# Kernel tuning notes

Measured on AMD Instinct MI355X. Metric: run time of the kernel, lower is better.

## Reference

```python
import jax, jax.numpy as jnp
import numpy as np

B, L, D = 4, 4096, 1024
H = 16
DK = D // H  # 64
EPS = 1e-5


def setup_inputs() -> dict:
    key = jax.random.key(0)
    ks = jax.random.split(key, 9)
    s = 1.0 / np.sqrt(D)
    return {
        "Q": jax.random.normal(ks[0], (B, L, D), dtype=jnp.float32),
        "W_Q": jax.random.uniform(ks[1], (D, D), jnp.float32, -s, s),
        "b_Q": jax.random.uniform(ks[2], (D,), jnp.float32, -s, s),
        "W_K": jax.random.uniform(ks[3], (D, D), jnp.float32, -s, s),
        "b_K": jax.random.uniform(ks[4], (D,), jnp.float32, -s, s),
        "W_V": jax.random.uniform(ks[5], (D, D), jnp.float32, -s, s),
        "b_V": jax.random.uniform(ks[6], (D,), jnp.float32, -s, s),
        "W_O": jax.random.uniform(ks[7], (D, D), jnp.float32, -s, s),
        "b_O": jax.random.uniform(ks[8], (D,), jnp.float32, -s, s),
    }


def reference(Q, W_Q, b_Q, W_K, b_K, W_V, b_V, W_O, b_O):
    # Projections (torch Linear: x @ W.T + b). K = V = Q (self-attention).
    q = (Q @ W_Q.T + b_Q).reshape(B, L, H, DK)  # blhd
    k = (Q @ W_K.T + b_K).reshape(B, L, H, DK)
    v = (Q @ W_V.T + b_V).reshape(B, L, H, DK)

    phi_q = jax.nn.elu(q) + 1.0
    phi_k = jax.nn.elu(k) + 1.0

    # KV outer-product accumulation over sequence: [b,h,d,m]
    KV = jnp.einsum('blhd,blhm->bhdm', phi_k, v)
    K_sum = phi_k.sum(axis=1)                       # [b,h,d]
    Z = 1.0 / (jnp.einsum('blhd,bhd->blh', phi_q, K_sum) + EPS)
    V_new = jnp.einsum('blhd,bhdm->blhm', phi_q, KV) * Z[..., None]

    out = V_new.reshape(B, L, H * DK) @ W_O.T + b_O  # [b,L,d_model]
    return out
```

## Files before the change

kernel.cpp:

```cpp
#include <hip/hip_runtime.h>

typedef unsigned short u16;
typedef unsigned int   u32;
typedef __attribute__((ext_vector_type(8))) short short8;
typedef __attribute__((ext_vector_type(4))) float f32x4;
typedef __attribute__((ext_vector_type(4))) u16   u16x4;

#define NB 4
#define SL 4096
#define DM 1024
#define NH 16
#define DK 64

__device__ __forceinline__ u16 f2bf(float f) {
  u32 u = __builtin_bit_cast(u32, f);
  u = (u + 0x7fffu + ((u >> 16) & 1u)) >> 16;
  return (u16)u;
}
__device__ __forceinline__ float bf2f(u16 v) {
  u32 u = ((u32)v) << 16;
  return __builtin_bit_cast(float, u);
}
__device__ __forceinline__ float eluP1(float x) {
  return x > 0.f ? x + 1.f : __expf(x);
}
#define GLL(gp, lp) __builtin_amdgcn_global_load_lds(     \
    (const __attribute__((address_space(1))) void*)(gp),  \
    (__attribute__((address_space(3))) void*)(lp), 16, 0, 0)

__global__ void cvt_all(const float* __restrict__ Qf,
                        const float* __restrict__ WQ, const float* __restrict__ WK,
                        const float* __restrict__ WV, const float* __restrict__ WO,
                        const float* __restrict__ bQ, const float* __restrict__ bK,
                        const float* __restrict__ bV,
                        u16* __restrict__ Qbf, u16* __restrict__ Wqkv,
                        u16* __restrict__ Wobf, float* __restrict__ biasQKV) {
  int b = blockIdx.x, tid = threadIdx.x;
  if (b < 16384) {
    int i = b * 256 + tid;
    f32x4 f = *(const f32x4*)(Qf + (size_t)i * 4);
    u16x4 o = { f2bf(f[0]), f2bf(f[1]), f2bf(f[2]), f2bf(f[3]) };
    *(u16x4*)(Qbf + (size_t)i * 4) = o;
  } else if (b < 20480) {
    int r = (b - 16384) >> 10;
    int i = ((b - 16384) & 1023) * 256 + tid;
    const float* src = r == 0 ? WQ : r == 1 ? WK : r == 2 ? WV : WO;
    u16* dst = (r == 3) ? Wobf : Wqkv + (size_t)r * 1048576;
    f32x4 f = *(const f32x4*)(src + (size_t)i * 4);
    u16x4 o = { f2bf(f[0]), f2bf(f[1]), f2bf(f[2]), f2bf(f[3]) };
    *(u16x4*)(dst + (size_t)i * 4) = o;
  } else {
    int i = (b - 20480) * 256 + tid;
    if (i < 3072) {
      float v = (i < 1024) ? bQ[i] : (i < 2048) ? bK[i - 1024] : bV[i - 2048];
      biasQKV[i] = v;
    }
  }
}


#define VM8 asm volatile("s_waitcnt vmcnt(8)" ::: "memory")

#define SA(buf, ks, kt) do {                                      \
    const u16* g_ = Ag + (((kt) & 15) * 64 + (ks) * 32);          \
    u16* l_ = ldsA + (buf) * 32768 + (ks) * 8192;                 \
    GLL(g_, l_); GLL(g_ + 16 * 1024, l_ + 512); } while (0)

#define SB(buf, ks, kt) do {                                      \
    const u16* g_ = Wg + (((kt) & 15) * 64 + (ks) * 32);          \
    u16* l_ = ldsB + (buf) * 32768 + (ks) * 8192;                 \
    GLL(g_, l_); GLL(g_ + 16 * 1024, l_ + 512); } while (0)

#define RD4(SET, buf, ks) do {                                    \
    const u16* pA_ = aBase + (buf) * 32768 + (ks) * 8192;         \
    _Pragma("unroll") for (int t_ = 0; t_ < 4; t_++)              \
      SET[t_] = *(const short8*)(pA_ + aOff[4 + t_]); } while (0)

#define RD8(ASET, BSET, buf, ks) do {                             \
    const u16* pA_ = aBase + (buf) * 32768 + (ks) * 8192;         \
    const u16* pB_ = bBase + (buf) * 32768 + (ks) * 8192;         \
    _Pragma("unroll") for (int t_ = 0; t_ < 4; t_++)              \
      ASET[t_] = *(const short8*)(pA_ + aOff[t_]);                \
    _Pragma("unroll") for (int u_ = 0; u_ < 4; u_++)              \
      BSET[u_] = *(const short8*)(pB_ + bOff[u_]); } while (0)

#define MFMA16(AF, BF, tb)                                        \
    _Pragma("unroll") for (int t_ = 0; t_ < 4; t_++) {            \
      acc[(tb) + t_][0] = __builtin_amdgcn_mfma_f32_16x16x32_bf16(AF[t_], BF[0], acc[(tb) + t_][0], 0, 0, 0); \
      acc[(tb) + t_][1] = __builtin_amdgcn_mfma_f32_16x16x32_bf16(AF[t_], BF[1], acc[(tb) + t_][1], 0, 0, 0); \
      acc[(tb) + t_][2] = __builtin_amdgcn_mfma_f32_16x16x32_bf16(AF[t_], BF[2], acc[(tb) + t_][2], 0, 0, 0); \
      acc[(tb) + t_][3] = __builtin_amdgcn_mfma_f32_16x16x32_bf16(AF[t_], BF[3], acc[(tb) + t_][3], 0, 0, 0); \
    }

#define PH(AFC, BFC, tb, RDOP, N, STG) do {                       \
    RDOP;                                                         \
    asm volatile("s_waitcnt lgkmcnt(" #N ")" ::: "memory");       \
    __builtin_amdgcn_sched_barrier(0);                            \
    __builtin_amdgcn_s_setprio(1);                                \
    MFMA16(AFC, BFC, tb);                                         \
    __builtin_amdgcn_s_setprio(0);                                \
    STG;                                                          \
    VM8;                                                          \
    __builtin_amdgcn_s_barrier();                                 \
  } while (0)

#define MAIN_8PHASE_LOOP                                          \
  short8 afA[4], afB[4], bfX[4], bfY[4];                          \
  SA(0, 0, 0); SB(0, 0, 0); SA(0, 1, 0); SB(0, 1, 0);             \
  SA(1, 0, 1); SB(1, 0, 1); SB(1, 1, 1);                          \
  VM8;                                                            \
  __builtin_amdgcn_s_barrier();                                   \
  asm volatile("" ::: "memory");                                  \
  RD8(afA, bfX, 0, 0);                                            \
  _Pragma("unroll 1")                                             \
  for (int i = 0; i < 8; i++) {                                   \
    PH(afA, bfX, 0, RD4(afB, 0, 0),        4, SA(1, 1, 2 * i + 1)); \
    PH(afB, bfX, 4, RD8(afA, bfY, 0, 1),   8, SB(0, 0, 2 * i + 2)); \
    PH(afA, bfY, 0, RD4(afB, 0, 1),        4, SA(0, 0, 2 * i + 2)); \
    PH(afB, bfY, 4, RD8(afA, bfX, 1, 0),   8, SB(0, 1, 2 * i + 2)); \
    PH(afA, bfX, 0, RD4(afB, 1, 0),        4, SA(0, 1, 2 * i + 2)); \
    PH(afB, bfX, 4, RD8(afA, bfY, 1, 1),   8, SB(1, 0, 2 * i + 3)); \
    PH(afA, bfY, 0, RD4(afB, 1, 1),        4, SA(1, 0, 2 * i + 3)); \
    PH(afB, bfY, 4, RD8(afA, bfX, 0, 0),   8, SB(1, 1, 2 * i + 3)); \
  }

__global__ __launch_bounds__(512, 2) void gemm_qkv(const u16* __restrict__ A,
                                                   const u16* __restrict__ Wqkv,
                                                   const float* __restrict__ biasQKV,
                                                   u16* __restrict__ phiq,
                                                   u16* __restrict__ phiKT,
                                                   u16* __restrict__ vT) {
  const int K = 1024;
  const int bId = blockIdx.x;
  const int xcd = bId & 7, s = bId >> 3;
  const int tile_m = xcd * 8 + s / 12;
  const int tile_n = s % 12;
  const int region = tile_n >> 2;

  const int tid = threadIdx.x, lane = tid & 63, wv = tid >> 6;
  const int i16 = lane & 15, q = lane >> 4;
  const int waveM = wv >> 2, waveN = wv & 3;

  __shared__ u16 smem[65536];

  const int r0 = wv * 32 + (lane >> 2);
  const int kc = (lane & 3) ^ ((r0 >> 1) & 3);
  const u16* Ag = A + (size_t)(tile_m * 256 + r0) * K + kc * 8;
  const u16* Wg = Wqkv + (size_t)(tile_n * 256 + r0) * K + kc * 8;
  u16* ldsA = smem + wv * 1024;
  u16* ldsB = smem + 16384 + wv * 1024;

  const u16* aBase = (region == 0) ? smem + 16384 : smem;
  const u16* bBase = (region == 0) ? smem : smem + 16384;
  int aOff[8], bOff[4];
#pragma unroll
  for (int t = 0; t < 8; t++) {
    int m = waveM * 128 + t * 16 + i16;
    aOff[t] = m * 32 + ((q ^ ((m >> 1) & 3)) << 3);
  }
#pragma unroll
  for (int u = 0; u < 4; u++) {
    int n = waveN * 64 + u * 16 + i16;
    bOff[u] = n * 32 + ((q ^ ((n >> 1) & 3)) << 3);
  }

  f32x4 acc[8][4] = {};

  MAIN_8PHASE_LOOP

  u16* T = smem;
  const int TS = 132;
  u16* dstT = (region == 1) ? phiKT : vT;
  const int bI = tile_m >> 4;
  const int lb = (tile_m & 15) * 256;

#pragma unroll
  for (int h = 0; h < 2; h++) {
    __syncthreads();
    if (waveM == h) {
      if (region == 0) {
#pragma unroll
        for (int t = 0; t < 8; t++) {
          f32x4 b4 = *(const f32x4*)(biasQKV + tile_n * 256 + h * 128 + t * 16 + q * 4);
#pragma unroll
          for (int u = 0; u < 4; u++) {
            int cC = waveN * 64 + u * 16 + i16;
            u16x4 o;
#pragma unroll
            for (int r = 0; r < 4; r++) o[r] = f2bf(eluP1(acc[t][u][r] + b4[r]));
            *(u16x4*)(T + cC * TS + t * 16 + q * 4) = o;
          }
        }
      } else {
#pragma unroll
        for (int u = 0; u < 4; u++) {
          int cC = waveN * 64 + u * 16 + i16;
          float bs = biasQKV[tile_n * 256 + cC];
#pragma unroll
          for (int t = 0; t < 8; t++) {
            u16x4 o;
#pragma unroll
            for (int r = 0; r < 4; r++) {
              float vv = acc[t][u][r] + bs;
              if (region == 1) vv = eluP1(vv);
              o[r] = f2bf(vv);
            }
            *(u16x4*)(T + cC * TS + t * 16 + q * 4) = o;
          }
        }
      }
    }
    __syncthreads();
    {
      const int Rl = tid >> 4, c16 = (tid & 15) * 8;
#pragma unroll
      for (int p = 0; p < 8; p++) {
        int R = p * 32 + Rl;
        short8 v8 = *(const short8*)(T + R * TS + c16);
        if (region == 0) {
          *(short8*)(phiq + (size_t)(tile_m * 256 + R) * DM + tile_n * 256 + h * 128 + c16) = v8;
        } else {
          int n_loc = tile_n * 256 + R - region * 1024;
          *(short8*)(dstT + ((size_t)bI * 1024 + n_loc) * 4096 + lb + h * 128 + c16) = v8;
        }
      }
    }
  }
}

__global__ __launch_bounds__(512, 2) void gemm_out(const u16* __restrict__ A,
                                                   const u16* __restrict__ W,
                                                   const float* __restrict__ bias,
                                                   float* __restrict__ outp) {
  const int K = 1024;
  const int bId = blockIdx.x;
  const int xcd = bId & 7, s = bId >> 3;
  const int tile_m = xcd * 8 + (s >> 2);
  const int tile_n = s & 3;

  const int tid = threadIdx.x, lane = tid & 63, wv = tid >> 6;
  const int i16 = lane & 15, q = lane >> 4;
  const int waveM = wv >> 2, waveN = wv & 3;

  __shared__ u16 smem[65536];

  const int r0 = wv * 32 + (lane >> 2);
  const int kc = (lane & 3) ^ ((r0 >> 1) & 3);
  const u16* Ag = A + (size_t)(tile_m * 256 + r0) * K + kc * 8;
  const u16* Wg = W + (size_t)(tile_n * 256 + r0) * K + kc * 8;
  u16* ldsA = smem + wv * 1024;
  u16* ldsB = smem + 16384 + wv * 1024;

  const u16* aBase = smem + 16384;
  const u16* bBase = smem;
  int aOff[8], bOff[4];
#pragma unroll
  for (int t = 0; t < 8; t++) {
    int m = waveM * 128 + t * 16 + i16;
    aOff[t] = m * 32 + ((q ^ ((m >> 1) & 3)) << 3);
  }
#pragma unroll
  for (int u = 0; u < 4; u++) {
    int n = waveN * 64 + u * 16 + i16;
    bOff[u] = n * 32 + ((q ^ ((n >> 1) & 3)) << 3);
  }

  f32x4 acc[8][4] = {};

  MAIN_8PHASE_LOOP

  float* Tf = (float*)smem;
  const int TFS = 68;
#pragma unroll
  for (int qn = 0; qn < 4; qn++) {
    __syncthreads();
    if (waveM == (qn >> 1)) {
      const int tb = (qn & 1) * 4;
#pragma unroll
      for (int tt = 0; tt < 4; tt++) {
        f32x4 b4 = *(const f32x4*)(bias + tile_n * 256 + qn * 64 + tt * 16 + q * 4);
#pragma unroll
        for (int u = 0; u < 4; u++) {
          int l = waveN * 64 + u * 16 + i16;
          f32x4 o;
#pragma unroll
          for (int r = 0; r < 4; r++) o[r] = acc[tb + tt][u][r] + b4[r];
          *(f32x4*)(Tf + l * TFS + tt * 16 + q * 4) = o;
        }
      }
    }
    __syncthreads();
    {
      const int Rl = tid >> 4, j = tid & 15;
#pragma unroll
      for (int p = 0; p < 8; p++) {
        int R = p * 32 + Rl;
        f32x4 v = *(const f32x4*)(Tf + R * TFS + j * 4);
        *(f32x4*)(outp + (size_t)(tile_m * 256 + R) * DM + tile_n * 256 + qn * 64 + j * 4) = v;
      }
    }
  }
}

__global__ __launch_bounds__(256) void kv_partial(const u16* __restrict__ phiKT,
                                                  const u16* __restrict__ vT,
                                                  float* __restrict__ part,
                                                  float* __restrict__ ksumP) {
  int bh = blockIdx.x >> 2, chunk = blockIdx.x & 3;
  int tid = threadIdx.x, lane = tid & 63, wv = tid >> 6;
  int i16 = lane & 15, q = lane >> 4;
  const u16* Ab = phiKT + (size_t)bh * DK * SL;
  const u16* Bb = vT + (size_t)bh * DK * SL;
  int l0 = (chunk * 4 + wv) * 256;
  f32x4 acc[4][4] = {};
  float ks[4] = {};
  for (int kk = 0; kk < 256; kk += 32) {
    int col = l0 + kk + q * 8;
    short8 af[4], bfr[4];
#pragma unroll
    for (int t = 0; t < 4; t++) af[t] = *(const short8*)(Ab + (size_t)(t * 16 + i16) * SL + col);
#pragma unroll
    for (int u = 0; u < 4; u++) bfr[u] = *(const short8*)(Bb + (size_t)(u * 16 + i16) * SL + col);
#pragma unroll
    for (int t = 0; t < 4; t++)
#pragma unroll
      for (int j = 0; j < 8; j++) ks[t] += bf2f((u16)af[t][j]);
#pragma unroll
    for (int t = 0; t < 4; t++)
#pragma unroll
      for (int u = 0; u < 4; u++)
        acc[t][u] = __builtin_amdgcn_mfma_f32_16x16x32_bf16(af[t], bfr[u], acc[t][u], 0, 0, 0);
  }
  __shared__ float red[4][64][64];
  __shared__ float ksl[4][4][64];
#pragma unroll
  for (int t = 0; t < 4; t++)
#pragma unroll
    for (int u = 0; u < 4; u++)
#pragma unroll
      for (int r = 0; r < 4; r++)
        red[wv][t * 16 + q * 4 + r][u * 16 + i16] = acc[t][u][r];
#pragma unroll
  for (int t = 0; t < 4; t++) ksl[wv][q][t * 16 + i16] = ks[t];
  __syncthreads();
  int d = tid >> 2, mg = (tid & 3) * 16;
#pragma unroll
  for (int c = 0; c < 4; c++) {
    int m = mg + c * 4;
    f32x4 o;
#pragma unroll
    for (int r = 0; r < 4; r++)
      o[r] = red[0][d][m + r] + red[1][d][m + r] + red[2][d][m + r] + red[3][d][m + r];
    *(f32x4*)(part + ((size_t)(chunk * 64 + bh) * 64 + d) * 64 + m) = o;
  }
  if (tid < 64) {
    float s = 0.f;
#pragma unroll
    for (int w2 = 0; w2 < 4; w2++)
#pragma unroll
      for (int q2 = 0; q2 < 4; q2++) s += ksl[w2][q2][tid];
    ksumP[chunk * 4096 + bh * 64 + tid] = s;
  }
}

__global__ __launch_bounds__(256) void kv_finalize(const float* __restrict__ part,
                                                   const float* __restrict__ ksumP,
                                                   u16* __restrict__ KVt,
                                                   float* __restrict__ Ksum) {
  int bh = blockIdx.x, tid = threadIdx.x;
  for (int e = tid; e < 4096; e += 256) {
    int d = e >> 6, m = e & 63;
    float s = part[((size_t)(0 * 64 + bh) * 64 + d) * 64 + m]
            + part[((size_t)(1 * 64 + bh) * 64 + d) * 64 + m]
            + part[((size_t)(2 * 64 + bh) * 64 + d) * 64 + m]
            + part[((size_t)(3 * 64 + bh) * 64 + d) * 64 + m];
    KVt[(size_t)bh * 4096 + m * 64 + d] = f2bf(s);
  }
  if (tid < 64) {
    float s = ksumP[0 * 4096 + bh * 64 + tid] + ksumP[1 * 4096 + bh * 64 + tid]
            + ksumP[2 * 4096 + bh * 64 + tid] + ksumP[3 * 4096 + bh * 64 + tid];
    Ksum[bh * 64 + tid] = s;
  }
}

__global__ __launch_bounds__(256) void vnew_kernel(const u16* __restrict__ phiq,
                                                   const u16* __restrict__ KVt,
                                                   const float* __restrict__ Ksum,
                                                   u16* __restrict__ Vnew) {
  int bh = blockIdx.x >> 5, lt = blockIdx.x & 31;
  int b = bh >> 4, h = bh & 15;
  int tid = threadIdx.x, lane = tid & 63, wv = tid >> 6;
  int i16 = lane & 15, q = lane >> 4;
  int waveM = wv & 1, waveL = wv >> 1;

  __shared__ u16 T[128 * 72];

  f32x4 ks00 = *(const f32x4*)(Ksum + bh * 64 + q * 8);
  f32x4 ks01 = *(const f32x4*)(Ksum + bh * 64 + q * 8 + 4);
  f32x4 ks10 = *(const f32x4*)(Ksum + bh * 64 + 32 + q * 8);
  f32x4 ks11 = *(const f32x4*)(Ksum + bh * 64 + 32 + q * 8 + 4);

  f32x4 acc[2][4] = {};
  float zp[4] = {0.f, 0.f, 0.f, 0.f};
#pragma unroll
  for (int step = 0; step < 2; step++) {
    int d0 = step * 32 + q * 8;
    short8 af[2], bfr[4];
#pragma unroll
    for (int t = 0; t < 2; t++) {
      int m = waveM * 32 + t * 16 + i16;
      af[t] = *(const short8*)(KVt + (size_t)bh * 4096 + m * 64 + d0);
    }
#pragma unroll
    for (int u = 0; u < 4; u++) {
      int l = lt * 128 + waveL * 64 + u * 16 + i16;
      bfr[u] = *(const short8*)(phiq + (size_t)(b * SL + l) * DM + h * 64 + d0);
      f32x4 k0 = step == 0 ? ks00 : ks10;
      f32x4 k1 = step == 0 ? ks01 : ks11;
#pragma unroll
      for (int j = 0; j < 4; j++) zp[u] += bf2f((u16)bfr[u][j]) * k0[j];
#pragma unroll
      for (int j = 0; j < 4; j++) zp[u] += bf2f((u16)bfr[u][4 + j]) * k1[j];
    }
#pragma unroll
    for (int t = 0; t < 2; t++)
#pragma unroll
      for (int u = 0; u < 4; u++)
        acc[t][u] = __builtin_amdgcn_mfma_f32_16x16x32_bf16(af[t], bfr[u], acc[t][u], 0, 0, 0);
  }

  float z[4];
#pragma unroll
  for (int u = 0; u < 4; u++) {
    float s = zp[u];
    s += __shfl_xor(s, 16);
    s += __shfl_xor(s, 32);
    z[u] = 1.0f / (s + 1e-5f);
  }

#pragma unroll
  for (int t = 0; t < 2; t++) {
#pragma unroll
    for (int u = 0; u < 4; u++) {
      int cI = waveL * 64 + u * 16 + i16;
      int nI = waveM * 32 + t * 16 + q * 4;
      u16x4 o;
#pragma unroll
      for (int r = 0; r < 4; r++) o[r] = f2bf(acc[t][u][r] * z[u]);
      *(u16x4*)(T + cI * 72 + nI) = o;
    }
  }
  __syncthreads();
  {
    const int Rl = tid >> 3, j = tid & 7;
#pragma unroll
    for (int p = 0; p < 4; p++) {
      int R = p * 32 + Rl;
      short8 v8 = *(const short8*)(T + R * 72 + j * 8);
      *(short8*)(Vnew + (size_t)(b * SL + lt * 128 + R) * DM + h * 64 + j * 8) = v8;
    }
  }
}

extern "C" void kernel_launch(void* const* d_in, const int* in_sizes, int n_in,
                              void* d_out, int out_size, void* d_ws, size_t ws_size,
                              hipStream_t stream) {
  const float* Qf = (const float*)d_in[0];
  const float* WQ = (const float*)d_in[1];
  const float* bQ = (const float*)d_in[2];
  const float* WK = (const float*)d_in[3];
  const float* bK = (const float*)d_in[4];
  const float* WV = (const float*)d_in[5];
  const float* bV = (const float*)d_in[6];
  const float* WO = (const float*)d_in[7];
  const float* bO = (const float*)d_in[8];

  const size_t MB = 1024ull * 1024ull;
  char* ws = (char*)d_ws;
  u16* Qbf     = (u16*)(ws + 0);
  u16* Vnew    = (u16*)(ws + 0);
  u16* Wqkv    = (u16*)(ws + 32 * MB);
  u16* Wobf    = (u16*)(ws + 38 * MB);
  float* biasQKV = (float*)(ws + 40 * MB);
  u16* phiq    = (u16*)(ws + 41 * MB);
  u16* phiKT   = (u16*)(ws + 73 * MB);
  u16* vT      = (u16*)(ws + 105 * MB);
  u16* KVt     = (u16*)(ws + 137 * MB);
  float* Ksum  = (float*)(ws + 138 * MB);
  float* part  = (float*)(ws + 139 * MB);
  float* ksumP = (float*)(ws + 143 * MB);

  cvt_all<<<20492, 256, 0, stream>>>(Qf, WQ, WK, WV, WO, bQ, bK, bV,
                                     Qbf, Wqkv, Wobf, biasQKV);

  gemm_qkv<<<768, 512, 0, stream>>>(Qbf, Wqkv, biasQKV, phiq, phiKT, vT);

  kv_partial<<<256, 256, 0, stream>>>(phiKT, vT, part, ksumP);
  kv_finalize<<<64, 256, 0, stream>>>(part, ksumP, KVt, Ksum);

  vnew_kernel<<<2048, 256, 0, stream>>>(phiq, KVt, Ksum, Vnew);

  gemm_out<<<256, 512, 0, stream>>>(Vnew, Wobf, bO, (float*)d_out);
}
```

Measured before the change: 334.2 us.

## Replace 8-phase GEMM pipeline with 4-slot LDS ring and one barrier per two k-tiles

Replaces the hand-scheduled 8-phase double-buffered main loop in both the QKV and output-projection GEMMs with a 4-slot ring of 32-wide k-tiles. Each iteration stages two tiles ahead, computes two tiles, then waits for all loads and issues a single barrier. The goal is fewer barriers and simpler scheduling. In exchange it drops the fine-grained lgkmcnt waits and sched_barrier interleaving, and vmcnt(0) forces a full drain of outstanding loads every iteration, which could expose memory latency.

```diff
diff --git a/kernel.cpp b/kernel.cpp
--- a/kernel.cpp
+++ b/kernel.cpp
@@ -59,30 +59,19 @@
 }
 
 
-#define VM8 asm volatile("s_waitcnt vmcnt(8)" ::: "memory")
-
-#define SA(buf, ks, kt) do {                                      \
-    const u16* g_ = Ag + (((kt) & 15) * 64 + (ks) * 32);          \
-    u16* l_ = ldsA + (buf) * 32768 + (ks) * 8192;                 \
+#define VM0 asm volatile("s_waitcnt vmcnt(0)" ::: "memory")
+
+#define SA(kt) do {                                               \
+    const u16* g_ = Ag + (((kt) & 31) * 32);                      \
+    u16* l_ = ldsA + (((kt) & 3) * 8192);                         \
     GLL(g_, l_); GLL(g_ + 16 * 1024, l_ + 512); } while (0)
 
-#define SB(buf, ks, kt) do {                                      \
-    const u16* g_ = Wg + (((kt) & 15) * 64 + (ks) * 32);          \
-    u16* l_ = ldsB + (buf) * 32768 + (ks) * 8192;                 \
+#define SB(kt) do {                                               \
+    const u16* g_ = Wg + (((kt) & 31) * 32);                      \
+    u16* l_ = ldsB + (((kt) & 3) * 8192);                         \
     GLL(g_, l_); GLL(g_ + 16 * 1024, l_ + 512); } while (0)
 
-#define RD4(SET, buf, ks) do {                                    \
-    const u16* pA_ = aBase + (buf) * 32768 + (ks) * 8192;         \
-    _Pragma("unroll") for (int t_ = 0; t_ < 4; t_++)              \
-      SET[t_] = *(const short8*)(pA_ + aOff[4 + t_]); } while (0)
-
-#define RD8(ASET, BSET, buf, ks) do {                             \
-    const u16* pA_ = aBase + (buf) * 32768 + (ks) * 8192;         \
-    const u16* pB_ = bBase + (buf) * 32768 + (ks) * 8192;         \
-    _Pragma("unroll") for (int t_ = 0; t_ < 4; t_++)              \
-      ASET[t_] = *(const short8*)(pA_ + aOff[t_]);                \
-    _Pragma("unroll") for (int u_ = 0; u_ < 4; u_++)              \
-      BSET[u_] = *(const short8*)(pB_ + bOff[u_]); } while (0)
+#define STG2(kt) do { SA(kt); SB(kt); } while (0)
 
 #define MFMA16(AF, BF, tb)                                        \
     _Pragma("unroll") for (int t_ = 0; t_ < 4; t_++) {            \
@@ -92,36 +81,36 @@
       acc[(tb) + t_][3] = __builtin_amdgcn_mfma_f32_16x16x32_bf16(AF[t_], BF[3], acc[(tb) + t_][3], 0, 0, 0); \
     }
 
-#define PH(AFC, BFC, tb, RDOP, N, STG) do {                       \
-    RDOP;                                                         \
-    asm volatile("s_waitcnt lgkmcnt(" #N ")" ::: "memory");       \
-    __builtin_amdgcn_sched_barrier(0);                            \
+#define TILE(buf) do {                                            \
+    short8 a0_[4], b_[4];                                         \
+    _Pragma("unroll") for (int t_ = 0; t_ < 4; t_++)              \
+      a0_[t_] = *(const short8*)(aBase + (buf) * 8192 + aOff[t_]);\
+    _Pragma("unroll") for (int u_ = 0; u_ < 4; u_++)              \
+      b_[u_] = *(const short8*)(bBase + (buf) * 8192 + bOff[u_]); \
     __builtin_amdgcn_s_setprio(1);                                \
-    MFMA16(AFC, BFC, tb);                                         \
+    MFMA16(a0_, b_, 0);                                           \
     __builtin_amdgcn_s_setprio(0);                                \
-    STG;                                                          \
-    VM8;                                                          \
-    __builtin_amdgcn_s_barrier();                                 \
+    short8 a4_[4];                                                \
+    _Pragma("unroll") for (int t_ = 0; t_ < 4; t_++)              \
+      a4_[t_] = *(const short8*)(aBase + (buf) * 8192 + aOff[4 + t_]); \
+    __builtin_amdgcn_s_setprio(1);                                \
+    MFMA16(a4_, b_, 4);                                           \
+    __builtin_amdgcn_s_setprio(0);                                \
   } while (0)
 
-#define MAIN_8PHASE_LOOP                                          \
-  short8 afA[4], afB[4], bfX[4], bfY[4];                          \
-  SA(0, 0, 0); SB(0, 0, 0); SA(0, 1, 0); SB(0, 1, 0);             \
-  SA(1, 0, 1); SB(1, 0, 1); SB(1, 1, 1);                          \
-  VM8;                                                            \
+#define MAIN_RING_LOOP                                            \
+  STG2(0); STG2(1);                                               \
+  VM0;                                                            \
   __builtin_amdgcn_s_barrier();                                   \
   asm volatile("" ::: "memory");                                  \
-  RD8(afA, bfX, 0, 0);                                            \
   _Pragma("unroll 1")                                             \
-  for (int i = 0; i < 8; i++) {                                   \
-    PH(afA, bfX, 0, RD4(afB, 0, 0),        4, SA(1, 1, 2 * i + 1)); \
-    PH(afB, bfX, 4, RD8(afA, bfY, 0, 1),   8, SB(0, 0, 2 * i + 2)); \
-    PH(afA, bfY, 0, RD4(afB, 0, 1),        4, SA(0, 0, 2 * i + 2)); \
-    PH(afB, bfY, 4, RD8(afA, bfX, 1, 0),   8, SB(0, 1, 2 * i + 2)); \
-    PH(afA, bfX, 0, RD4(afB, 1, 0),        4, SA(0, 1, 2 * i + 2)); \
-    PH(afB, bfX, 4, RD8(afA, bfY, 1, 1),   8, SB(1, 0, 2 * i + 3)); \
-    PH(afA, bfY, 0, RD4(afB, 1, 1),        4, SA(1, 0, 2 * i + 3)); \
-    PH(afB, bfY, 4, RD8(afA, bfX, 0, 0),   8, SB(1, 1, 2 * i + 3)); \
+  for (int kt = 0; kt < 32; kt += 2) {                            \
+    STG2(kt + 2);                                                 \
+    TILE(kt & 3);                                                 \
+    STG2(kt + 3);                                                 \
+    TILE((kt + 1) & 3);                                           \
+    VM0;                                                          \
+    __builtin_amdgcn_s_barrier();                                 \
   }
 
 __global__ __launch_bounds__(512, 2) void gemm_qkv(const u16* __restrict__ A,
@@ -148,10 +137,10 @@
   const u16* Ag = A + (size_t)(tile_m * 256 + r0) * K + kc * 8;
   const u16* Wg = Wqkv + (size_t)(tile_n * 256 + r0) * K + kc * 8;
   u16* ldsA = smem + wv * 1024;
-  u16* ldsB = smem + 16384 + wv * 1024;
-
-  const u16* aBase = (region == 0) ? smem + 16384 : smem;
-  const u16* bBase = (region == 0) ? smem : smem + 16384;
+  u16* ldsB = smem + 32768 + wv * 1024;
+
+  const u16* aBase = (region == 0) ? smem + 32768 : smem;
+  const u16* bBase = (region == 0) ? smem : smem + 32768;
   int aOff[8], bOff[4];
 #pragma unroll
   for (int t = 0; t < 8; t++) {
@@ -166,7 +155,7 @@
 
   f32x4 acc[8][4] = {};
 
-  MAIN_8PHASE_LOOP
+  MAIN_RING_LOOP
 
   u16* T = smem;
   const int TS = 132;
@@ -249,9 +238,9 @@
   const u16* Ag = A + (size_t)(tile_m * 256 + r0) * K + kc * 8;
   const u16* Wg = W + (size_t)(tile_n * 256 + r0) * K + kc * 8;
   u16* ldsA = smem + wv * 1024;
-  u16* ldsB = smem + 16384 + wv * 1024;
-
-  const u16* aBase = smem + 16384;
+  u16* ldsB = smem + 32768 + wv * 1024;
+
+  const u16* aBase = smem + 32768;
   const u16* bBase = smem;
   int aOff[8], bOff[4];
 #pragma unroll
@@ -267,7 +256,7 @@
 
   f32x4 acc[8][4] = {};
 
-  MAIN_8PHASE_LOOP
+  MAIN_RING_LOOP
 
   float* Tf = (float*)smem;
   const int TFS = 68;
```

After: 326.3 us. -2.4%, faster.
